# Kernel tuning notes

Measured on AMD Instinct MI355X. Metric: run time of the kernel, lower is better.

## Reference

```python
import jax, jax.numpy as jnp
import numpy as np

VOCAB = 50257
HIDDEN = 16
B, T = 256, 8192


def setup_inputs() -> dict:
    key = jax.random.key(0)
    ks = jax.random.split(key, 8)
    seq = jax.random.randint(ks[0], (B, T), 0, VOCAB, dtype=jnp.int64 if jax.config.jax_enable_x64 else jnp.int32)
    s = 1.0 / np.sqrt(HIDDEN)
    return {
        "seq": seq,
        "embed": jax.random.normal(ks[1], (VOCAB, HIDDEN), jnp.float32) * 0.02,
        # nn.Linear(hidden, 1): weight [1,hidden] -> stored transposed [hidden,1]
        "Wg": jax.random.uniform(ks[2], (HIDDEN, 1), jnp.float32, -s, s),
        "bg": jax.random.uniform(ks[3], (1,), jnp.float32, -s, s),
        # nn.Linear(hidden, hidden) -> [hidden, hidden] (transposed)
        "Wu": jax.random.uniform(ks[4], (HIDDEN, HIDDEN), jnp.float32, -s, s),
        "bu": jax.random.uniform(ks[5], (HIDDEN,), jnp.float32, -s, s),
        # nn.Linear(hidden, vocab) -> [hidden, vocab] (transposed)
        "Wo": jax.random.uniform(ks[6], (HIDDEN, VOCAB), jnp.float32, -s, s),
        "bo": jax.random.uniform(ks[7], (VOCAB,), jnp.float32, -s, s),
    }


def reference(seq, embed, Wg, bg, Wu, bu, Wo, bo):
    # The torch loop is a purely additive recurrence:
    #   memory = sum_t sigmoid(gate(x_t)) * tanh(update(x_t))
    # so we batch all timesteps and do one masked-free sum over T.
    x = embed[seq]                                  # [B, T, H] gather
    g = jax.nn.sigmoid(jnp.einsum("bth,ho->bto", x, Wg) + bg)   # [B, T, 1]
    new_content = jnp.tanh(jnp.einsum("bth,hk->btk", x, Wu) + bu)  # [B, T, H]
    memory = jnp.sum(g * new_content, axis=1)       # [B, H]
    return memory @ Wo + bo                         # [B, vocab]
```

## Files before the change

### kernel.cpp

```cpp
#include <hip/hip_runtime.h>
#include <cmath>

#define VOCAB   50257
#define HIDDEN  16
#define BATCH   256
#define SEQLEN  8192
#define TCHUNKS 4
#define K3_BCHUNK 64

__global__ __launch_bounds__(256) void k1_build_table(
    const float* __restrict__ embed, const float* __restrict__ Wg,
    const float* __restrict__ bg,    const float* __restrict__ Wu,
    const float* __restrict__ bu,    float* __restrict__ ctab)
{
    __shared__ float sWu[256], sWg[16], sbu[16];
    const int tid = threadIdx.x;
    sWu[tid] = Wu[tid];
    if (tid < 16) { sWg[tid] = Wg[tid]; sbu[tid] = bu[tid]; }
    __syncthreads();

    const int v = blockIdx.x * 256 + tid;
    if (v >= VOCAB) return;

    const float4* er = (const float4*)(embed + (size_t)v * HIDDEN);
    float4 e0 = er[0], e1 = er[1], e2 = er[2], e3 = er[3];
    float e[16] = {e0.x,e0.y,e0.z,e0.w, e1.x,e1.y,e1.z,e1.w,
                   e2.x,e2.y,e2.z,e2.w, e3.x,e3.y,e3.z,e3.w};

    float z = bg[0];
#pragma unroll
    for (int h = 0; h < 16; ++h) z = fmaf(e[h], sWg[h], z);
    const float g = 1.0f / (1.0f + __expf(-z));

    float o[16];
#pragma unroll
    for (int k = 0; k < 16; ++k) {
        float u = sbu[k];
#pragma unroll
        for (int h = 0; h < 16; ++h) u = fmaf(e[h], sWu[h * 16 + k], u);
        o[k] = g * tanhf(u);
    }

    float4* cr = (float4*)(ctab + (size_t)v * HIDDEN);
    cr[0] = make_float4(o[0],  o[1],  o[2],  o[3]);
    cr[1] = make_float4(o[4],  o[5],  o[6],  o[7]);
    cr[2] = make_float4(o[8],  o[9],  o[10], o[11]);
    cr[3] = make_float4(o[12], o[13], o[14], o[15]);
}

__global__ __launch_bounds__(256) void k2_accum(
    const int* __restrict__ seq, const float* __restrict__ ctab,
    float* __restrict__ partial)
{
    const int b = blockIdx.x, chunk = blockIdx.y, tid = threadIdx.x;
    const int TPC = SEQLEN / TCHUNKS;
    const int* srow = seq + (size_t)b * SEQLEN + chunk * TPC;

    float r[16];
#pragma unroll
    for (int k = 0; k < 16; ++k) r[k] = 0.f;

#pragma unroll
    for (int i = 0; i < TPC / 256; ++i) {
        const int idx = srow[i * 256 + tid];
        const float4* cr = (const float4*)(ctab + (size_t)idx * HIDDEN);
        float4 c0 = cr[0], c1 = cr[1], c2 = cr[2], c3 = cr[3];
        r[0]+=c0.x;  r[1]+=c0.y;  r[2]+=c0.z;  r[3]+=c0.w;
        r[4]+=c1.x;  r[5]+=c1.y;  r[6]+=c1.z;  r[7]+=c1.w;
        r[8]+=c2.x;  r[9]+=c2.y;  r[10]+=c2.z; r[11]+=c2.w;
        r[12]+=c3.x; r[13]+=c3.y; r[14]+=c3.z; r[15]+=c3.w;
    }

#pragma unroll
    for (int off = 32; off > 0; off >>= 1)
#pragma unroll
        for (int k = 0; k < 16; ++k) r[k] += __shfl_xor(r[k], off, 64);

    __shared__ float red[4][16];
    const int lane = tid & 63, wave = tid >> 6;
    if (lane == 0) {
#pragma unroll
        for (int k = 0; k < 16; ++k) red[wave][k] = r[k];
    }
    __syncthreads();
    if (tid < 16) {
        const float s = red[0][tid] + red[1][tid] + red[2][tid] + red[3][tid];
        partial[((size_t)chunk * BATCH + b) * HIDDEN + tid] = s;
    }
}

__global__ __launch_bounds__(256) void k3_output(
    const float* __restrict__ partial, const float* __restrict__ Wo,
    const float* __restrict__ bo,      float* __restrict__ out)
{
    __shared__ float smem[K3_BCHUNK * 16];
    const int tid = threadIdx.x;
    const int b0 = blockIdx.y * K3_BCHUNK;

#pragma unroll
    for (int i = tid; i < K3_BCHUNK * 16; i += 256) {
        const int bl = i >> 4, h = i & 15;
        float s = 0.f;
#pragma unroll
        for (int ch = 0; ch < TCHUNKS; ++ch)
            s += partial[((size_t)ch * BATCH + (b0 + bl)) * HIDDEN + h];
        smem[i] = s;
    }
    __syncthreads();

    const int v = blockIdx.x * 256 + tid;
    if (v >= VOCAB) return;

    float w[16];
#pragma unroll
    for (int h = 0; h < 16; ++h) w[h] = Wo[(size_t)h * VOCAB + v];
    const float bias = bo[v];

    float* orow = out + (size_t)b0 * VOCAB + v;
#pragma unroll 4
    for (int bl = 0; bl < K3_BCHUNK; ++bl) {
        float acc = bias;
#pragma unroll
        for (int h = 0; h < 16; ++h)
            acc = fmaf(smem[bl * 16 + h], w[h], acc);
        orow[(size_t)bl * VOCAB] = acc;
    }
}

extern "C" void kernel_launch(void* const* d_in, const int* in_sizes, int n_in,
                              void* d_out, int out_size, void* d_ws, size_t ws_size,
                              hipStream_t stream) {
    const int*   seq   = (const int*)  d_in[0];
    const float* embed = (const float*)d_in[1];
    const float* Wg    = (const float*)d_in[2];
    const float* bg    = (const float*)d_in[3];
    const float* Wu    = (const float*)d_in[4];
    const float* bu    = (const float*)d_in[5];
    const float* Wo    = (const float*)d_in[6];
    const float* bo    = (const float*)d_in[7];
    float* out = (float*)d_out;

    float* ctab    = (float*)d_ws;
    float* partial = ctab + (size_t)VOCAB * HIDDEN;

    k1_build_table<<<dim3((VOCAB + 255) / 256), 256, 0, stream>>>(
        embed, Wg, bg, Wu, bu, ctab);
    k2_accum<<<dim3(BATCH, TCHUNKS), 256, 0, stream>>>(seq, ctab, partial);
    k3_output<<<dim3((VOCAB + 255) / 256, BATCH / K3_BCHUNK), 256, 0, stream>>>(
        partial, Wo, bo, out);
}
```

Measured before the change: 133.0 us.

## Split each gathered row across four lanes and double sequence chunks

The accumulation kernel now gives each table row to four threads, each loading one float4, instead of one thread loading all four float4s. This makes the gather loads better coalesced and cuts per-thread registers from 16 accumulators to 4. The reduction keeps the per-component lanes separate and writes them out from lanes 0-3. The number of sequence chunks doubles, giving more blocks for parallelism, at the cost of more partials for the output kernel to sum.

New measurement: 120.0 us. 1.11x faster.

```diff
diff --git a/kernel.cpp b/kernel.cpp
--- a/kernel.cpp
+++ b/kernel.cpp
@@ -5,7 +5,7 @@
 #define HIDDEN  16
 #define BATCH   256
 #define SEQLEN  8192
-#define TCHUNKS 4
+#define TCHUNKS 8
 #define K3_BCHUNK 64
 
 __global__ __launch_bounds__(256) void k1_build_table(
@@ -53,39 +53,39 @@
     float* __restrict__ partial)
 {
     const int b = blockIdx.x, chunk = blockIdx.y, tid = threadIdx.x;
-    const int TPC = SEQLEN / TCHUNKS;
-    const int* srow = seq + (size_t)b * SEQLEN + chunk * TPC;
+    constexpr int TPC = SEQLEN / TCHUNKS;
+    const int* srow = seq + (size_t)b * SEQLEN + (size_t)chunk * TPC;
+    const int sub = tid & 3;
+    const int tok = tid >> 2;
 
-    float r[16];
+    float rx = 0.f, ry = 0.f, rz = 0.f, rw = 0.f;
 #pragma unroll
-    for (int k = 0; k < 16; ++k) r[k] = 0.f;
-
-#pragma unroll
-    for (int i = 0; i < TPC / 256; ++i) {
-        const int idx = srow[i * 256 + tid];
-        const float4* cr = (const float4*)(ctab + (size_t)idx * HIDDEN);
-        float4 c0 = cr[0], c1 = cr[1], c2 = cr[2], c3 = cr[3];
-        r[0]+=c0.x;  r[1]+=c0.y;  r[2]+=c0.z;  r[3]+=c0.w;
-        r[4]+=c1.x;  r[5]+=c1.y;  r[6]+=c1.z;  r[7]+=c1.w;
-        r[8]+=c2.x;  r[9]+=c2.y;  r[10]+=c2.z; r[11]+=c2.w;
-        r[12]+=c3.x; r[13]+=c3.y; r[14]+=c3.z; r[15]+=c3.w;
+    for (int i = 0; i < TPC / 64; ++i) {
+        const int idx = srow[i * 64 + tok];
+        const float4 c = ((const float4*)(ctab + (size_t)idx * HIDDEN))[sub];
+        rx += c.x; ry += c.y; rz += c.z; rw += c.w;
     }
 
 #pragma unroll
-    for (int off = 32; off > 0; off >>= 1)
-#pragma unroll
-        for (int k = 0; k < 16; ++k) r[k] += __shfl_xor(r[k], off, 64);
+    for (int off = 4; off < 64; off <<= 1) {
+        rx += __shfl_xor(rx, off, 64);
+        ry += __shfl_xor(ry, off, 64);
+        rz += __shfl_xor(rz, off, 64);
+        rw += __shfl_xor(rw, off, 64);
+    }
 
     __shared__ float red[4][16];
     const int lane = tid & 63, wave = tid >> 6;
-    if (lane == 0) {
-#pragma unroll
-        for (int k = 0; k < 16; ++k) red[wave][k] = r[k];
+    if (lane < 4) {
+        red[wave][lane * 4 + 0] = rx;
+        red[wave][lane * 4 + 1] = ry;
+        red[wave][lane * 4 + 2] = rz;
+        red[wave][lane * 4 + 3] = rw;
     }
     __syncthreads();
     if (tid < 16) {
-        const float s = red[0][tid] + red[1][tid] + red[2][tid] + red[3][tid];
-        partial[((size_t)chunk * BATCH + b) * HIDDEN + tid] = s;
+        partial[((size_t)chunk * BATCH + b) * HIDDEN + tid] =
+            red[0][tid] + red[1][tid] + red[2][tid] + red[3][tid];
     }
 }
 
```
